# Kernel tuning notes

Measured on AMD Instinct MI355X. Metric: run time of the kernel, lower is better.

Reference implementation:

```python
import jax, jax.numpy as jnp
import numpy as np

HID = 256
IN_DIM = 256
OUT_DIM = 10
L_CYCLES = 6
H_CYCLES = 3
BATCH = 131072
LN_EPS = 1e-5


def _layernorm(v, w, b):
    mu = jnp.mean(v, axis=-1, keepdims=True)
    var = jnp.mean(jnp.square(v - mu), axis=-1, keepdims=True)
    return (v - mu) * jax.lax.rsqrt(var + LN_EPS) * w + b


def setup_inputs() -> dict:
    key = jax.random.key(0)
    ks = jax.random.split(key, 12)
    s = lambda fan_in: 1.0 / np.sqrt(fan_in)
    inp = {
        "x": jax.random.normal(ks[0], (BATCH, IN_DIM), dtype=jnp.float32),
        "W_in": jax.random.uniform(ks[1], (IN_DIM, HID), jnp.float32, -s(IN_DIM), s(IN_DIM)),
        "b_in": jnp.zeros((HID,), jnp.float32),
        "y_init": jax.random.normal(ks[2], (1, HID), dtype=jnp.float32) * 0.02,
        "W_up": jax.random.uniform(ks[3], (HID, 4 * HID), jnp.float32, -s(HID), s(HID)),
        "b_up": jnp.zeros((4 * HID,), jnp.float32),
        "W_down": jax.random.uniform(ks[4], (4 * HID, HID), jnp.float32, -s(4 * HID), s(4 * HID)),
        "b_down": jnp.zeros((HID,), jnp.float32),
        "ln_w": jnp.ones((HID,), jnp.float32),
        "ln_b": jnp.zeros((HID,), jnp.float32),
        "W_comb": jax.random.uniform(ks[5], (2 * HID, HID), jnp.float32, -s(2 * HID), s(2 * HID)),
        "b_comb": jnp.zeros((HID,), jnp.float32),
        "W_yt": jax.random.uniform(ks[6], (HID, HID), jnp.float32, -s(HID), s(HID)),
        "b_yt": jnp.zeros((HID,), jnp.float32),
        "W_head": jax.random.uniform(ks[7], (HID, OUT_DIM), jnp.float32, -s(HID), s(HID)),
        "b_head": jnp.zeros((OUT_DIM,), jnp.float32),
    }
    return inp


def reference(x, W_in, b_in, y_init, W_up, b_up, W_down, b_down, ln_w, ln_b,
              W_comb, b_comb, W_yt, b_yt, W_head, b_head):
    z = x @ W_in + b_in                      # [B, H]
    y = jnp.broadcast_to(y_init, (x.shape[0], HID))
    for _ in range(H_CYCLES):
        for _ in range(L_CYCLES):
            h = jax.nn.gelu(z @ W_up + b_up, approximate=False)
            h = h @ W_down + b_down
            z = _layernorm(z + h, ln_w, ln_b)
        combined = jnp.concatenate([z, y], axis=-1)   # [B, 2H]
        h = jax.nn.gelu(combined @ W_comb + b_comb, approximate=False)
        y = y + h @ W_yt + b_yt
    return y @ W_head + b_head
```

## Files before the change

### kernel.cpp

```cpp
#include <hip/hip_runtime.h>

typedef _Float16 h16;
typedef h16 h16x8 __attribute__((ext_vector_type(8)));
typedef float f32x4 __attribute__((ext_vector_type(4)));

#define MFMA16(a, b, c) __builtin_amdgcn_mfma_f32_16x16x32_f16(a, b, c, 0, 0, 0)

typedef __attribute__((address_space(1))) const char gconst_char;
typedef __attribute__((address_space(3))) char lds_char;
#define GL_LDS16(g, l) __builtin_amdgcn_global_load_lds((gconst_char*)(g), (lds_char*)(l), 16, 0, 0)

#define WIN_OFF   0
#define WIN_CSH   17408
#define WUP_OFF   (WIN_OFF + 8 * WIN_CSH)
#define WUP_CSH   17408
#define WDN_OFF   (WUP_OFF + 32 * WUP_CSH)
#define WDN_CSH   20480
#define WCOMB_OFF (WDN_OFF + 32 * WDN_CSH)
#define WCOMB_CSH 33792
#define WYT_OFF   (WCOMB_OFF + 8 * WCOMB_CSH)
#define WYT_CSH   20480
#define WHEAD_OFF (WYT_OFF + 8 * WYT_CSH)
#define WHEAD_SZ  9216
#define ZY_OFF    (WHEAD_OFF + WHEAD_SZ)
#define ZY_BYTES  (131072UL * 512UL * 2UL)

#define L_WUP0 0
#define L_WUP1 17408
#define L_WDN0 34816
#define L_WDN1 55296
#define L_HS   75776
#define L_BUP  96256
#define L_BDN  100352
#define L_LNW  101376
#define L_LNB  102400
#define SMEM_MEGA 103424

#define C_WC0 0
#define C_WC1 33792
#define C_WY0 67584
#define C_WY1 88064
#define C_GS  108544
#define C_BC  129024
#define C_BY  130048
#define SMEM_COMB 131072

#define SMEM_HEAD 9216

__device__ __forceinline__ void stage_calls(const char* src, char* dst, int calls, int wave,
                                            int nw, int lane) {
  for (int i = wave; i < calls; i += nw)
    GL_LDS16(src + i * 1024 + lane * 16, dst + i * 1024);
}

__device__ __forceinline__ float gelu_f(float x) {
  float t = x * (1.5957691216f + 0.0713548354f * x * x);
  float e = __expf(-t);
  return x * __builtin_amdgcn_rcpf(1.0f + e);
}

__global__ void prepA_kernel(const float* __restrict__ src, h16* __restrict__ dst,
                             int K, int KPp, int CHN, int Nsrc, int CSHh, int tot) {
  for (int d = blockIdx.x * 256 + threadIdx.x; d < tot; d += gridDim.x * 256) {
    int chunk = d / CSHh, r = d % CSHh;
    float v = 0.0f;
    if (r < CHN * KPp) {
      int nl = r / KPp, k = r % KPp;
      int n = chunk * CHN + nl;
      if (k < K && n < Nsrc) v = src[(long)k * Nsrc + n];
    }
    dst[d] = (h16)v;
  }
}
__global__ void prepB_kernel(const float* __restrict__ src, h16* __restrict__ dst,
                             int Kc, int KP2p, int N, int CSHh, int tot) {
  for (int d = blockIdx.x * 256 + threadIdx.x; d < tot; d += gridDim.x * 256) {
    int chunk = d / CSHh, r = d % CSHh;
    float v = 0.0f;
    if (r < N * KP2p) {
      int n = r / KP2p, kp = r % KP2p;
      if (kp < Kc) v = src[(long)(chunk * Kc + kp) * N + n];
    }
    dst[d] = (h16)v;
  }
}

__global__ __launch_bounds__(512) void mega_kernel(
    const float* x, h16* zy,
    const char* __restrict__ winP, const char* __restrict__ wupP, const char* __restrict__ wdnP,
    const float* __restrict__ b_in, const float* __restrict__ b_up,
    const float* __restrict__ b_down, const float* __restrict__ ln_w,
    const float* __restrict__ ln_b, int first) {
  extern __shared__ char smem[];
  const int tid = threadIdx.x, wave = tid >> 6, lane = tid & 63;
  const int q = lane >> 4, c = lane & 15;
  const long m0 = (long)blockIdx.x * 256 + wave * 32;

  float* bupL = (float*)(smem + L_BUP);
  float* bdnL = (float*)(smem + L_BDN);
  float* lnwL = (float*)(smem + L_LNW);
  float* lnbL = (float*)(smem + L_LNB);
  for (int i = tid; i < 1024; i += 512) bupL[i] = b_up[i];
  if (tid < 256) { bdnL[tid] = b_down[tid]; lnwL[tid] = ln_w[tid]; lnbL[tid] = ln_b[tid]; }

  f32x4 acc2[2][16];
  h16x8 az[2][8];
  h16* hsH = (h16*)(smem + L_HS + wave * 2560);
  const f32x4 vzero = {0.0f, 0.0f, 0.0f, 0.0f};

  if (first) {
#pragma unroll
    for (int rt = 0; rt < 2; ++rt)
#pragma unroll
      for (int kk = 0; kk < 8; ++kk) {
        const float* p = x + (m0 + rt * 16 + c) * 256 + kk * 32 + q * 8;
        f32x4 u0 = *(const f32x4*)p;
        f32x4 u1 = *(const f32x4*)(p + 4);
        h16x8 a;
        a[0] = (h16)u0[0]; a[1] = (h16)u0[1]; a[2] = (h16)u0[2]; a[3] = (h16)u0[3];
        a[4] = (h16)u1[0]; a[5] = (h16)u1[1]; a[6] = (h16)u1[2]; a[7] = (h16)u1[3];
        az[rt][kk] = a;
      }
#pragma unroll
    for (int rt = 0; rt < 2; ++rt)
#pragma unroll
      for (int nt = 0; nt < 16; ++nt) acc2[rt][nt] = vzero;

    stage_calls(winP, smem + L_WUP0, 17, wave, 8, lane);
    __syncthreads();
#pragma unroll
    for (int ncI = 0; ncI < 8; ++ncI) {
      if (ncI < 7)
        stage_calls(winP + (ncI + 1) * WIN_CSH, smem + (((ncI + 1) & 1) ? L_WUP1 : L_WUP0),
                    17, wave, 8, lane);
      const char* wb = smem + ((ncI & 1) ? L_WUP1 : L_WUP0);
#pragma unroll
      for (int kk = 0; kk < 8; ++kk)
#pragma unroll
        for (int nt = 0; nt < 2; ++nt) {
          h16x8 b = *(const h16x8*)(wb + ((nt * 16 + c) * 264 + kk * 32 + q * 8) * 2);
#pragma unroll
          for (int rt = 0; rt < 2; ++rt)
            acc2[rt][ncI * 2 + nt] = MFMA16(az[rt][kk], b, acc2[rt][ncI * 2 + nt]);
        }
      __syncthreads();
    }
#pragma unroll
    for (int nt = 0; nt < 16; ++nt) {
      float bi = b_in[nt * 16 + c];
#pragma unroll
      for (int rt = 0; rt < 2; ++rt)
#pragma unroll
        for (int r = 0; r < 4; ++r) acc2[rt][nt][r] += bi;
    }
  } else {
#pragma unroll
    for (int rt = 0; rt < 2; ++rt)
#pragma unroll
      for (int kk = 0; kk < 8; ++kk)
        az[rt][kk] = *(const h16x8*)(zy + (m0 + rt * 16 + c) * 512 + kk * 32 + q * 8);
#pragma unroll
    for (int rt = 0; rt < 2; ++rt)
#pragma unroll
      for (int nt = 0; nt < 16; ++nt)
#pragma unroll
        for (int r = 0; r < 4; ++r)
          acc2[rt][nt][r] = (float)zy[(m0 + rt * 16 + q * 4 + r) * 512 + nt * 16 + c];
  }

  for (int it = 0; it < 6; ++it) {
    if (it > 0 || first) {
      h16* zth = (h16*)(smem + wave * 8448);
#pragma unroll
      for (int rt = 0; rt < 2; ++rt) {
#pragma unroll
        for (int nt = 0; nt < 16; ++nt)
#pragma unroll
          for (int r = 0; r < 4; ++r)
            zth[(q * 4 + r) * 264 + nt * 16 + c] = (h16)acc2[rt][nt][r];
#pragma unroll
        for (int kk = 0; kk < 8; ++kk)
          az[rt][kk] = *(const h16x8*)(zth + c * 264 + kk * 32 + q * 8);
      }
    }
    __syncthreads();
    stage_calls(wupP, smem + L_WUP0, 17, wave, 8, lane);
    stage_calls(wdnP, smem + L_WDN0, 20, wave, 8, lane);
    __syncthreads();

    for (int nc = 0; nc < 32; ++nc) {
      if (nc < 31) {
        int nb = (nc + 1) & 1;
        stage_calls(wupP + (nc + 1) * WUP_CSH, smem + (nb ? L_WUP1 : L_WUP0), 17, wave, 8, lane);
        stage_calls(wdnP + (nc + 1) * WDN_CSH, smem + (nb ? L_WDN1 : L_WDN0), 20, wave, 8, lane);
      }
      const char* wub = smem + ((nc & 1) ? L_WUP1 : L_WUP0);
      const char* wdb = smem + ((nc & 1) ? L_WDN1 : L_WDN0);

      f32x4 acc1[2][2];
      acc1[0][0] = vzero; acc1[0][1] = vzero; acc1[1][0] = vzero; acc1[1][1] = vzero;
#pragma unroll
      for (int kk = 0; kk < 8; ++kk)
#pragma unroll
        for (int nt = 0; nt < 2; ++nt) {
          h16x8 b = *(const h16x8*)(wub + ((nt * 16 + c) * 264 + kk * 32 + q * 8) * 2);
#pragma unroll
          for (int rt = 0; rt < 2; ++rt) acc1[rt][nt] = MFMA16(az[rt][kk], b, acc1[rt][nt]);
        }
#pragma unroll
      for (int rt = 0; rt < 2; ++rt)
#pragma unroll
        for (int nt = 0; nt < 2; ++nt) {
          float bu = bupL[nc * 32 + nt * 16 + c];
#pragma unroll
          for (int r = 0; r < 4; ++r) {
            float g = gelu_f(acc1[rt][nt][r] + bu);
            hsH[(rt * 16 + q * 4 + r) * 40 + nt * 16 + c] = (h16)g;
          }
        }
      h16x8 ah[2];
#pragma unroll
      for (int rt = 0; rt < 2; ++rt)
        ah[rt] = *(const h16x8*)(hsH + (rt * 16 + c) * 40 + q * 8);
#pragma unroll
      for (int nt = 0; nt < 16; ++nt) {
        h16x8 b = *(const h16x8*)(wdb + ((nt * 16 + c) * 40 + q * 8) * 2);
#pragma unroll
        for (int rt = 0; rt < 2; ++rt) acc2[rt][nt] = MFMA16(ah[rt], b, acc2[rt][nt]);
      }
      __syncthreads();
    }

#pragma unroll
    for (int rt = 0; rt < 2; ++rt) {
      float sum[4] = {0, 0, 0, 0}, sq[4] = {0, 0, 0, 0};
#pragma unroll
      for (int nt = 0; nt < 16; ++nt) {
        float bd = bdnL[nt * 16 + c];
#pragma unroll
        for (int r = 0; r < 4; ++r) {
          float v = acc2[rt][nt][r] + bd;
          acc2[rt][nt][r] = v;
          sum[r] += v;
          sq[r] += v * v;
        }
      }
#pragma unroll
      for (int r = 0; r < 4; ++r)
#pragma unroll
        for (int m = 1; m < 16; m <<= 1) {
          sum[r] += __shfl_xor(sum[r], m, 16);
          sq[r] += __shfl_xor(sq[r], m, 16);
        }
      float mu[4], rs[4];
#pragma unroll
      for (int r = 0; r < 4; ++r) {
        mu[r] = sum[r] * (1.0f / 256.0f);
        float var = sq[r] * (1.0f / 256.0f) - mu[r] * mu[r];
        rs[r] = __builtin_amdgcn_rsqf(var + 1e-5f);
      }
#pragma unroll
      for (int nt = 0; nt < 16; ++nt) {
        float w = lnwL[nt * 16 + c], bb = lnbL[nt * 16 + c];
#pragma unroll
        for (int r = 0; r < 4; ++r)
          acc2[rt][nt][r] = (acc2[rt][nt][r] - mu[r]) * rs[r] * w + bb;
      }
    }
  }

#pragma unroll
  for (int rt = 0; rt < 2; ++rt)
#pragma unroll
    for (int nt = 0; nt < 16; ++nt)
#pragma unroll
      for (int r = 0; r < 4; ++r)
        zy[(m0 + rt * 16 + q * 4 + r) * 512 + nt * 16 + c] = (h16)acc2[rt][nt][r];
}

__global__ __launch_bounds__(512) void comb_kernel(
    h16* zy, const char* __restrict__ wcP, const char* __restrict__ wytP,
    const float* __restrict__ b_comb, const float* __restrict__ b_yt,
    const float* __restrict__ y_init, int first) {
  extern __shared__ char smem[];
  const int tid = threadIdx.x, wave = tid >> 6, lane = tid & 63;
  const int q = lane >> 4, c = lane & 15;
  const long m0 = (long)blockIdx.x * 256 + wave * 32;

  float* bcL = (float*)(smem + C_BC);
  float* byL = (float*)(smem + C_BY);
  if (tid < 256) { bcL[tid] = b_comb[tid]; byL[tid] = b_yt[tid]; }

  f32x4 acc2[2][16];
  if (first) {
#pragma unroll
    for (int nt = 0; nt < 16; ++nt) {
      float yv = y_init[nt * 16 + c];
#pragma unroll
      for (int rt = 0; rt < 2; ++rt)
#pragma unroll
        for (int r = 0; r < 4; ++r) acc2[rt][nt][r] = yv;
    }
  } else {
#pragma unroll
    for (int rt = 0; rt < 2; ++rt)
#pragma unroll
      for (int nt = 0; nt < 16; ++nt)
#pragma unroll
        for (int r = 0; r < 4; ++r)
          acc2[rt][nt][r] = (float)zy[(m0 + rt * 16 + q * 4 + r) * 512 + 256 + nt * 16 + c];
  }
  h16* gsH = (h16*)(smem + C_GS + wave * 2560);
  const f32x4 vzero = {0.0f, 0.0f, 0.0f, 0.0f};

  stage_calls(wcP, smem + C_WC0, 33, wave, 8, lane);
  stage_calls(wytP, smem + C_WY0, 20, wave, 8, lane);
  __syncthreads();

  for (int nc = 0; nc < 8; ++nc) {
    if (nc < 7) {
      int nb = (nc + 1) & 1;
      stage_calls(wcP + (nc + 1) * WCOMB_CSH, smem + (nb ? C_WC1 : C_WC0), 33, wave, 8, lane);
      stage_calls(wytP + (nc + 1) * WYT_CSH, smem + (nb ? C_WY1 : C_WY0), 20, wave, 8, lane);
    }
    const char* wcb = smem + ((nc & 1) ? C_WC1 : C_WC0);
    const char* wyb = smem + ((nc & 1) ? C_WY1 : C_WY0);

    f32x4 acc1[2][2];
    acc1[0][0] = vzero; acc1[0][1] = vzero; acc1[1][0] = vzero; acc1[1][1] = vzero;
#pragma unroll
    for (int kk = 0; kk < 16; ++kk) {
      h16x8 a[2];
#pragma unroll
      for (int rt = 0; rt < 2; ++rt)
        a[rt] = *(const h16x8*)(zy + (m0 + rt * 16 + c) * 512 + kk * 32 + q * 8);
#pragma unroll
      for (int nt = 0; nt < 2; ++nt) {
        h16x8 b = *(const h16x8*)(wcb + ((nt * 16 + c) * 520 + kk * 32 + q * 8) * 2);
#pragma unroll
        for (int rt = 0; rt < 2; ++rt) acc1[rt][nt] = MFMA16(a[rt], b, acc1[rt][nt]);
      }
    }
#pragma unroll
    for (int rt = 0; rt < 2; ++rt)
#pragma unroll
      for (int nt = 0; nt < 2; ++nt) {
        float bc = bcL[nc * 32 + nt * 16 + c];
#pragma unroll
        for (int r = 0; r < 4; ++r) {
          float g = gelu_f(acc1[rt][nt][r] + bc);
          gsH[(rt * 16 + q * 4 + r) * 40 + nt * 16 + c] = (h16)g;
        }
      }
    h16x8 ah[2];
#pragma unroll
    for (int rt = 0; rt < 2; ++rt)
      ah[rt] = *(const h16x8*)(gsH + (rt * 16 + c) * 40 + q * 8);
#pragma unroll
    for (int nt = 0; nt < 16; ++nt) {
      h16x8 b = *(const h16x8*)(wyb + ((nt * 16 + c) * 40 + q * 8) * 2);
#pragma unroll
      for (int rt = 0; rt < 2; ++rt) acc2[rt][nt] = MFMA16(ah[rt], b, acc2[rt][nt]);
    }
    __syncthreads();
  }

#pragma unroll
  for (int nt = 0; nt < 16; ++nt) {
    float by = byL[nt * 16 + c];
#pragma unroll
    for (int rt = 0; rt < 2; ++rt)
#pragma unroll
      for (int r = 0; r < 4; ++r)
        zy[(m0 + rt * 16 + q * 4 + r) * 512 + 256 + nt * 16 + c] = (h16)(acc2[rt][nt][r] + by);
  }
}

__global__ __launch_bounds__(256) void head_kernel(const h16* zy, const char* __restrict__ whP,
                                                   const float* __restrict__ b_head,
                                                   float* __restrict__ out) {
  extern __shared__ char smem[];
  const int tid = threadIdx.x, wave = tid >> 6, lane = tid & 63;
  const int q = lane >> 4, c = lane & 15;
  const long m0 = (long)blockIdx.x * 128 + wave * 32;

  stage_calls(whP, smem, 9, wave, 4, lane);
  __syncthreads();

  f32x4 acc[2];
  const f32x4 vzero = {0.0f, 0.0f, 0.0f, 0.0f};
  acc[0] = vzero; acc[1] = vzero;
#pragma unroll
  for (int kk = 0; kk < 8; ++kk) {
    h16x8 b = *(const h16x8*)(smem + (c * 264 + kk * 32 + q * 8) * 2);
#pragma unroll
    for (int rt = 0; rt < 2; ++rt) {
      h16x8 a = *(const h16x8*)(zy + (m0 + rt * 16 + c) * 512 + 256 + kk * 32 + q * 8);
      acc[rt] = MFMA16(a, b, acc[rt]);
    }
  }
  if (c < 10) {
    float bh = b_head[c];
#pragma unroll
    for (int rt = 0; rt < 2; ++rt)
#pragma unroll
      for (int r = 0; r < 4; ++r)
        out[(m0 + rt * 16 + q * 4 + r) * 10 + c] = acc[rt][r] + bh;
  }
}

extern "C" void kernel_launch(void* const* d_in, const int* in_sizes, int n_in, void* d_out,
                              int out_size, void* d_ws, size_t ws_size, hipStream_t stream) {
  (void)in_sizes; (void)n_in; (void)out_size;
  const float* x      = (const float*)d_in[0];
  const float* W_in   = (const float*)d_in[1];
  const float* b_in   = (const float*)d_in[2];
  const float* y_init = (const float*)d_in[3];
  const float* W_up   = (const float*)d_in[4];
  const float* b_up   = (const float*)d_in[5];
  const float* W_down = (const float*)d_in[6];
  const float* b_down = (const float*)d_in[7];
  const float* ln_w   = (const float*)d_in[8];
  const float* ln_b   = (const float*)d_in[9];
  const float* W_comb = (const float*)d_in[10];
  const float* b_comb = (const float*)d_in[11];
  const float* W_yt   = (const float*)d_in[12];
  const float* b_yt   = (const float*)d_in[13];
  const float* W_head = (const float*)d_in[14];
  const float* b_head = (const float*)d_in[15];

  char* ws = (char*)d_ws;
  h16* winP   = (h16*)(ws + WIN_OFF);
  h16* wupP   = (h16*)(ws + WUP_OFF);
  h16* wdnP   = (h16*)(ws + WDN_OFF);
  h16* wcombP = (h16*)(ws + WCOMB_OFF);
  h16* wytP   = (h16*)(ws + WYT_OFF);
  h16* wheadP = (h16*)(ws + WHEAD_OFF);
  h16* zy = (ws_size >= (size_t)ZY_OFF + ZY_BYTES) ? (h16*)(ws + ZY_OFF) : (h16*)d_in[0];

  hipFuncSetAttribute((const void*)mega_kernel, hipFuncAttributeMaxDynamicSharedMemorySize,
                      SMEM_MEGA);
  hipFuncSetAttribute((const void*)comb_kernel, hipFuncAttributeMaxDynamicSharedMemorySize,
                      SMEM_COMB);

  {
    int tot;
    tot = 8 * (WIN_CSH / 2);
    prepA_kernel<<<dim3((tot + 255) / 256), dim3(256), 0, stream>>>(W_in, winP, 256, 264, 32, 256, WIN_CSH / 2, tot);
    tot = 32 * (WUP_CSH / 2);
    prepA_kernel<<<dim3((tot + 255) / 256), dim3(256), 0, stream>>>(W_up, wupP, 256, 264, 32, 1024, WUP_CSH / 2, tot);
    tot = 8 * (WCOMB_CSH / 2);
    prepA_kernel<<<dim3((tot + 255) / 256), dim3(256), 0, stream>>>(W_comb, wcombP, 512, 520, 32, 256, WCOMB_CSH / 2, tot);
    tot = WHEAD_SZ / 2;
    prepA_kernel<<<dim3((tot + 255) / 256), dim3(256), 0, stream>>>(W_head, wheadP, 256, 264, 16, 10, WHEAD_SZ / 2, tot);
    tot = 32 * (WDN_CSH / 2);
    prepB_kernel<<<dim3((tot + 255) / 256), dim3(256), 0, stream>>>(W_down, wdnP, 32, 40, 256, WDN_CSH / 2, tot);
    tot = 8 * (WYT_CSH / 2);
    prepB_kernel<<<dim3((tot + 255) / 256), dim3(256), 0, stream>>>(W_yt, wytP, 32, 40, 256, WYT_CSH / 2, tot);
  }

  for (int h = 0; h < 3; ++h) {
    mega_kernel<<<dim3(512), dim3(512), SMEM_MEGA, stream>>>(
        x, zy, (const char*)winP, (const char*)wupP, (const char*)wdnP, b_in, b_up, b_down,
        ln_w, ln_b, (h == 0) ? 1 : 0);
    comb_kernel<<<dim3(512), dim3(512), SMEM_COMB, stream>>>(
        zy, (const char*)wcombP, (const char*)wytP, b_comb, b_yt, y_init, (h == 0) ? 1 : 0);
  }
  head_kernel<<<dim3(1024), dim3(256), SMEM_HEAD, stream>>>(zy, (const char*)wheadP, b_head,
                                                            (float*)d_out);
}
```

Before: 4.068 ms.

## Pre-swizzle weights into MFMA fragment order and pipeline staging across iterations

```diff
diff --git a/kernel.cpp b/kernel.cpp
--- a/kernel.cpp
+++ b/kernel.cpp
@@ -10,42 +10,43 @@
 typedef __attribute__((address_space(3))) char lds_char;
 #define GL_LDS16(g, l) __builtin_amdgcn_global_load_lds((gconst_char*)(g), (lds_char*)(l), 16, 0, 0)
 
+#define WIN_CSH   16384
 #define WIN_OFF   0
-#define WIN_CSH   17408
-#define WUP_OFF   (WIN_OFF + 8 * WIN_CSH)
-#define WUP_CSH   17408
-#define WDN_OFF   (WUP_OFF + 32 * WUP_CSH)
-#define WDN_CSH   20480
-#define WCOMB_OFF (WDN_OFF + 32 * WDN_CSH)
-#define WCOMB_CSH 33792
-#define WYT_OFF   (WCOMB_OFF + 8 * WCOMB_CSH)
-#define WYT_CSH   20480
-#define WHEAD_OFF (WYT_OFF + 8 * WYT_CSH)
-#define WHEAD_SZ  9216
-#define ZY_OFF    (WHEAD_OFF + WHEAD_SZ)
+#define WUP_CSH   16384
+#define WUP_OFF   131072
+#define WDN_CSH   16384
+#define WDN_OFF   655360
+#define WCOMB_CSH 32768
+#define WCOMB_OFF 1179648
+#define WYT_CSH   16384
+#define WYT_OFF   1441792
+#define WHEAD_SZ  8192
+#define WHEAD_OFF 1572864
+#define ZY_OFF    1581056
 #define ZY_BYTES  (131072UL * 512UL * 2UL)
 
 #define L_WUP0 0
-#define L_WUP1 17408
-#define L_WDN0 34816
-#define L_WDN1 55296
-#define L_HS   75776
-#define L_BUP  96256
-#define L_BDN  100352
-#define L_LNW  101376
-#define L_LNB  102400
-#define SMEM_MEGA 103424
+#define L_WUP1 16384
+#define L_WDN0 32768
+#define L_WDN1 49152
+#define L_HS   65536
+#define L_ZT   86016
+#define L_BUP  153600
+#define L_BDN  157696
+#define L_LNW  158720
+#define L_LNB  159744
+#define SMEM_MEGA 160768
 
 #define C_WC0 0
-#define C_WC1 33792
-#define C_WY0 67584
-#define C_WY1 88064
-#define C_GS  108544
-#define C_BC  129024
-#define C_BY  130048
-#define SMEM_COMB 131072
-
-#define SMEM_HEAD 9216
+#define C_WC1 32768
+#define C_WY0 65536
+#define C_WY1 81920
+#define C_GS  98304
+#define C_BC  118784
+#define C_BY  119808
+#define SMEM_COMB 120832
+
+#define SMEM_HEAD 8192
 
 __device__ __forceinline__ void stage_calls(const char* src, char* dst, int calls, int wave,
                                             int nw, int lane) {
@@ -59,29 +60,32 @@
   return x * __builtin_amdgcn_rcpf(1.0f + e);
 }
 
-__global__ void prepA_kernel(const float* __restrict__ src, h16* __restrict__ dst,
-                             int K, int KPp, int CHN, int Nsrc, int CSHh, int tot) {
+__global__ void prepC_kernel(const float* __restrict__ src, h16* __restrict__ dst,
+                             int Nsrc, int CSHh, int tot) {
   for (int d = blockIdx.x * 256 + threadIdx.x; d < tot; d += gridDim.x * 256) {
     int chunk = d / CSHh, r = d % CSHh;
-    float v = 0.0f;
-    if (r < CHN * KPp) {
-      int nl = r / KPp, k = r % KPp;
-      int n = chunk * CHN + nl;
-      if (k < K && n < Nsrc) v = src[(long)k * Nsrc + n];
-    }
-    dst[d] = (h16)v;
-  }
-}
-__global__ void prepB_kernel(const float* __restrict__ src, h16* __restrict__ dst,
-                             int Kc, int KP2p, int N, int CSHh, int tot) {
+    int frag = r >> 9, lane = (r >> 3) & 63, j = r & 7;
+    int kk = frag >> 1, nt = frag & 1, q = lane >> 4, c = lane & 15;
+    int k = kk * 32 + q * 8 + j;
+    int n = chunk * 32 + nt * 16 + c;
+    dst[d] = (h16)src[(long)k * Nsrc + n];
+  }
+}
+__global__ void prepD_kernel(const float* __restrict__ src, h16* __restrict__ dst, int tot) {
   for (int d = blockIdx.x * 256 + threadIdx.x; d < tot; d += gridDim.x * 256) {
-    int chunk = d / CSHh, r = d % CSHh;
-    float v = 0.0f;
-    if (r < N * KP2p) {
-      int n = r / KP2p, kp = r % KP2p;
-      if (kp < Kc) v = src[(long)(chunk * Kc + kp) * N + n];
-    }
-    dst[d] = (h16)v;
+    int chunk = d >> 13, r = d & 8191;
+    int nt = r >> 9, lane = (r >> 3) & 63, j = r & 7;
+    int q = lane >> 4, c = lane & 15;
+    int k = chunk * 32 + q * 8 + j;
+    dst[d] = (h16)src[(long)k * 256 + nt * 16 + c];
+  }
+}
+__global__ void prepH_kernel(const float* __restrict__ src, h16* __restrict__ dst) {
+  for (int d = blockIdx.x * 256 + threadIdx.x; d < 4096; d += gridDim.x * 256) {
+    int kk = d >> 9, lane = (d >> 3) & 63, j = d & 7;
+    int q = lane >> 4, c = lane & 15;
+    int k = kk * 32 + q * 8 + j;
+    dst[d] = (h16)((c < 10) ? src[k * 10 + c] : 0.0f);
   }
 }
 
@@ -90,10 +94,11 @@
     const char* __restrict__ winP, const char* __restrict__ wupP, const char* __restrict__ wdnP,
     const float* __restrict__ b_in, const float* __restrict__ b_up,
     const float* __restrict__ b_down, const float* __restrict__ ln_w,
-    const float* __restrict__ ln_b, int first) {
+    const float* __restrict__ ln_b, const float* __restrict__ y_init, int first) {
   extern __shared__ char smem[];
   const int tid = threadIdx.x, wave = tid >> 6, lane = tid & 63;
   const int q = lane >> 4, c = lane & 15;
+  const int lane16 = lane << 4;
   const long m0 = (long)blockIdx.x * 256 + wave * 32;
 
   float* bupL = (float*)(smem + L_BUP);
@@ -106,6 +111,7 @@
   f32x4 acc2[2][16];
   h16x8 az[2][8];
   h16* hsH = (h16*)(smem + L_HS + wave * 2560);
+  h16* zth = (h16*)(smem + L_ZT + wave * 8448);
   const f32x4 vzero = {0.0f, 0.0f, 0.0f, 0.0f};
 
   if (first) {
@@ -126,22 +132,21 @@
 #pragma unroll
       for (int nt = 0; nt < 16; ++nt) acc2[rt][nt] = vzero;
 
-    stage_calls(winP, smem + L_WUP0, 17, wave, 8, lane);
+    stage_calls(winP, smem + L_WUP0, 16, wave, 8, lane);
     __syncthreads();
 #pragma unroll
     for (int ncI = 0; ncI < 8; ++ncI) {
       if (ncI < 7)
         stage_calls(winP + (ncI + 1) * WIN_CSH, smem + (((ncI + 1) & 1) ? L_WUP1 : L_WUP0),
-                    17, wave, 8, lane);
+                    16, wave, 8, lane);
       const char* wb = smem + ((ncI & 1) ? L_WUP1 : L_WUP0);
 #pragma unroll
       for (int kk = 0; kk < 8; ++kk)
 #pragma unroll
         for (int nt = 0; nt < 2; ++nt) {
-          h16x8 b = *(const h16x8*)(wb + ((nt * 16 + c) * 264 + kk * 32 + q * 8) * 2);
-#pragma unroll
-          for (int rt = 0; rt < 2; ++rt)
-            acc2[rt][ncI * 2 + nt] = MFMA16(az[rt][kk], b, acc2[rt][ncI * 2 + nt]);
+          h16x8 b = *(const h16x8*)(wb + ((kk * 2 + nt) << 10) + lane16);
+          acc2[0][ncI * 2 + nt] = MFMA16(az[0][kk], b, acc2[0][ncI * 2 + nt]);
+          acc2[1][ncI * 2 + nt] = MFMA16(az[1][kk], b, acc2[1][ncI * 2 + nt]);
         }
       __syncthreads();
     }
@@ -153,24 +158,43 @@
 #pragma unroll
         for (int r = 0; r < 4; ++r) acc2[rt][nt][r] += bi;
     }
+#pragma unroll
+    for (int kk = 0; kk < 8; ++kk) {
+      const float* p = y_init + kk * 32 + q * 8;
+      f32x4 u0 = *(const f32x4*)p;
+      f32x4 u1 = *(const f32x4*)(p + 4);
+      h16x8 a;
+      a[0] = (h16)u0[0]; a[1] = (h16)u0[1]; a[2] = (h16)u0[2]; a[3] = (h16)u0[3];
+      a[4] = (h16)u1[0]; a[5] = (h16)u1[1]; a[6] = (h16)u1[2]; a[7] = (h16)u1[3];
+#pragma unroll
+      for (int rt = 0; rt < 2; ++rt)
+        *(h16x8*)(zy + (m0 + rt * 16 + c) * 512 + 256 + kk * 32 + q * 8) = a;
+    }
+    stage_calls(wupP, smem + L_WUP0, 16, wave, 8, lane);
+    stage_calls(wdnP, smem + L_WDN0, 16, wave, 8, lane);
   } else {
+    stage_calls(wupP, smem + L_WUP0, 16, wave, 8, lane);
+    stage_calls(wdnP, smem + L_WDN0, 16, wave, 8, lane);
 #pragma unroll
     for (int rt = 0; rt < 2; ++rt)
 #pragma unroll
       for (int kk = 0; kk < 8; ++kk)
         az[rt][kk] = *(const h16x8*)(zy + (m0 + rt * 16 + c) * 512 + kk * 32 + q * 8);
 #pragma unroll
-    for (int rt = 0; rt < 2; ++rt)
+    for (int rt = 0; rt < 2; ++rt) {
+#pragma unroll
+      for (int kk = 0; kk < 8; ++kk)
+        *(h16x8*)(zth + c * 264 + kk * 32 + q * 8) = az[rt][kk];
 #pragma unroll
       for (int nt = 0; nt < 16; ++nt)
 #pragma unroll
         for (int r = 0; r < 4; ++r)
-          acc2[rt][nt][r] = (float)zy[(m0 + rt * 16 + q * 4 + r) * 512 + nt * 16 + c];
+          acc2[rt][nt][r] = (float)zth[(q * 4 + r) * 264 + nt * 16 + c];
+    }
   }
 
   for (int it = 0; it < 6; ++it) {
     if (it > 0 || first) {
-      h16* zth = (h16*)(smem + wave * 8448);
 #pragma unroll
       for (int rt = 0; rt < 2; ++rt) {
 #pragma unroll
@@ -183,19 +207,19 @@
           az[rt][kk] = *(const h16x8*)(zth + c * 264 + kk * 32 + q * 8);
       }
     }
-    __syncthreads();
-    stage_calls(wupP, smem + L_WUP0, 17, wave, 8, lane);
-    stage_calls(wdnP, smem + L_WDN0, 20, wave, 8, lane);
-    __syncthreads();
 
     for (int nc = 0; nc < 32; ++nc) {
-      if (nc < 31) {
-        int nb = (nc + 1) & 1;
-        stage_calls(wupP + (nc + 1) * WUP_CSH, smem + (nb ? L_WUP1 : L_WUP0), 17, wave, 8, lane);
-        stage_calls(wdnP + (nc + 1) * WDN_CSH, smem + (nb ? L_WDN1 : L_WDN0), 20, wave, 8, lane);
-      }
-      const char* wub = smem + ((nc & 1) ? L_WUP1 : L_WUP0);
-      const char* wdb = smem + ((nc & 1) ? L_WDN1 : L_WDN0);
+      const int tc = it * 32 + nc;
+      __syncthreads();
+      if (tc < 191) {
+        const int nxt = (nc + 1) & 31;
+        char* wu = smem + (((tc + 1) & 1) ? L_WUP1 : L_WUP0);
+        char* wd = smem + (((tc + 1) & 1) ? L_WDN1 : L_WDN0);
+        stage_calls(wupP + nxt * WUP_CSH, wu, 16, wave, 8, lane);
+        stage_calls(wdnP + nxt * WDN_CSH, wd, 16, wave, 8, lane);
+      }
+      const char* wub = smem + ((tc & 1) ? L_WUP1 : L_WUP0);
+      const char* wdb = smem + ((tc & 1) ? L_WDN1 : L_WDN0);
 
       f32x4 acc1[2][2];
       acc1[0][0] = vzero; acc1[0][1] = vzero; acc1[1][0] = vzero; acc1[1][1] = vzero;
@@ -203,9 +227,9 @@
       for (int kk = 0; kk < 8; ++kk)
 #pragma unroll
         for (int nt = 0; nt < 2; ++nt) {
-          h16x8 b = *(const h16x8*)(wub + ((nt * 16 + c) * 264 + kk * 32 + q * 8) * 2);
-#pragma unroll
-          for (int rt = 0; rt < 2; ++rt) acc1[rt][nt] = MFMA16(az[rt][kk], b, acc1[rt][nt]);
+          h16x8 b = *(const h16x8*)(wub + ((kk * 2 + nt) << 10) + lane16);
+          acc1[0][nt] = MFMA16(az[0][kk], b, acc1[0][nt]);
+          acc1[1][nt] = MFMA16(az[1][kk], b, acc1[1][nt]);
         }
 #pragma unroll
       for (int rt = 0; rt < 2; ++rt)
@@ -218,17 +242,14 @@
             hsH[(rt * 16 + q * 4 + r) * 40 + nt * 16 + c] = (h16)g;
           }
         }
-      h16x8 ah[2];
-#pragma unroll
-      for (int rt = 0; rt < 2; ++rt)
-        ah[rt] = *(const h16x8*)(hsH + (rt * 16 + c) * 40 + q * 8);
+      h16x8 ah0 = *(const h16x8*)(hsH + c * 40 + q * 8);
+      h16x8 ah1 = *(const h16x8*)(hsH + (16 + c) * 40 + q * 8);
 #pragma unroll
       for (int nt = 0; nt < 16; ++nt) {
-        h16x8 b = *(const h16x8*)(wdb + ((nt * 16 + c) * 40 + q * 8) * 2);
-#pragma unroll
-        for (int rt = 0; rt < 2; ++rt) acc2[rt][nt] = MFMA16(ah[rt], b, acc2[rt][nt]);
-      }
-      __syncthreads();
+        h16x8 b = *(const h16x8*)(wdb + (nt << 10) + lane16);
+        acc2[0][nt] = MFMA16(ah0, b, acc2[0][nt]);
+        acc2[1][nt] = MFMA16(ah1, b, acc2[1][nt]);
+      }
     }
 
 #pragma unroll
@@ -270,12 +291,17 @@
   }
 
 #pragma unroll
-  for (int rt = 0; rt < 2; ++rt)
+  for (int rt = 0; rt < 2; ++rt) {
 #pragma unroll
     for (int nt = 0; nt < 16; ++nt)
 #pragma unroll
       for (int r = 0; r < 4; ++r)
-        zy[(m0 + rt * 16 + q * 4 + r) * 512 + nt * 16 + c] = (h16)acc2[rt][nt][r];
+        zth[(q * 4 + r) * 264 + nt * 16 + c] = (h16)acc2[rt][nt][r];
+#pragma unroll
+    for (int kk = 0; kk < 8; ++kk)
+      *(h16x8*)(zy + (m0 + rt * 16 + c) * 512 + kk * 32 + q * 8) =
+          *(const h16x8*)(zth + c * 264 + kk * 32 + q * 8);
+  }
 }
 
 __global__ __launch_bounds__(512) void comb_kernel(
@@ -285,6 +311,7 @@
   extern __shared__ char smem[];
   const int tid = threadIdx.x, wave = tid >> 6, lane = tid & 63;
   const int q = lane >> 4, c = lane & 15;
+  const int lane16 = lane << 4;
   const long m0 = (long)blockIdx.x * 256 + wave * 32;
 
   float* bcL = (float*)(smem + C_BC);
@@ -302,26 +329,34 @@
         for (int r = 0; r < 4; ++r) acc2[rt][nt][r] = yv;
     }
   } else {
-#pragma unroll
-    for (int rt = 0; rt < 2; ++rt)
+    h16* zth = (h16*)(smem + wave * 8448);
+#pragma unroll
+    for (int rt = 0; rt < 2; ++rt) {
+#pragma unroll
+      for (int kk = 0; kk < 8; ++kk)
+        *(h16x8*)(zth + c * 264 + kk * 32 + q * 8) =
+            *(const h16x8*)(zy + (m0 + rt * 16 + c) * 512 + 256 + kk * 32 + q * 8);
 #pragma unroll
       for (int nt = 0; nt < 16; ++nt)
 #pragma unroll
         for (int r = 0; r < 4; ++r)
-          acc2[rt][nt][r] = (float)zy[(m0 + rt * 16 + q * 4 + r) * 512 + 256 + nt * 16 + c];
-  }
+          acc2[rt][nt][r] = (float)zth[(q * 4 + r) * 264 + nt * 16 + c];
+    }
+  }
+  __syncthreads();
+
   h16* gsH = (h16*)(smem + C_GS + wave * 2560);
   const f32x4 vzero = {0.0f, 0.0f, 0.0f, 0.0f};
 
-  stage_calls(wcP, smem + C_WC0, 33, wave, 8, lane);
-  stage_calls(wytP, smem + C_WY0, 20, wave, 8, lane);
-  __syncthreads();
+  stage_calls(wcP, smem + C_WC0, 32, wave, 8, lane);
+  stage_calls(wytP, smem + C_WY0, 16, wave, 8, lane);
 
   for (int nc = 0; nc < 8; ++nc) {
+    __syncthreads();
     if (nc < 7) {
       int nb = (nc + 1) & 1;
-      stage_calls(wcP + (nc + 1) * WCOMB_CSH, smem + (nb ? C_WC1 : C_WC0), 33, wave, 8, lane);
-      stage_calls(wytP + (nc + 1) * WYT_CSH, smem + (nb ? C_WY1 : C_WY0), 20, wave, 8, lane);
+      stage_calls(wcP + (nc + 1) * WCOMB_CSH, smem + (nb ? C_WC1 : C_WC0), 32, wave, 8, lane);
+      stage_calls(wytP + (nc + 1) * WYT_CSH, smem + (nb ? C_WY1 : C_WY0), 16, wave, 8, lane);
     }
     const char* wcb = smem + ((nc & 1) ? C_WC1 : C_WC0);
     const char* wyb = smem + ((nc & 1) ? C_WY1 : C_WY0);
@@ -330,15 +365,13 @@
     acc1[0][0] = vzero; acc1[0][1] = vzero; acc1[1][0] = vzero; acc1[1][1] = vzero;
 #pragma unroll
     for (int kk = 0; kk < 16; ++kk) {
-      h16x8 a[2];
-#pragma unroll
-      for (int rt = 0; rt < 2; ++rt)
-        a[rt] = *(const h16x8*)(zy + (m0 + rt * 16 + c) * 512 + kk * 32 + q * 8);
+      h16x8 a0 = *(const h16x8*)(zy + (m0 + c) * 512 + kk * 32 + q * 8);
+      h16x8 a1 = *(const h16x8*)(zy + (m0 + 16 + c) * 512 + kk * 32 + q * 8);
 #pragma unroll
       for (int nt = 0; nt < 2; ++nt) {
-        h16x8 b = *(const h16x8*)(wcb + ((nt * 16 + c) * 520 + kk * 32 + q * 8) * 2);
-#pragma unroll
-        for (int rt = 0; rt < 2; ++rt) acc1[rt][nt] = MFMA16(a[rt], b, acc1[rt][nt]);
+        h16x8 b = *(const h16x8*)(wcb + ((kk * 2 + nt) << 10) + lane16);
+        acc1[0][nt] = MFMA16(a0, b, acc1[0][nt]);
+        acc1[1][nt] = MFMA16(a1, b, acc1[1][nt]);
       }
     }
 #pragma unroll
@@ -352,27 +385,31 @@
           gsH[(rt * 16 + q * 4 + r) * 40 + nt * 16 + c] = (h16)g;
         }
       }
-    h16x8 ah[2];
-#pragma unroll
-    for (int rt = 0; rt < 2; ++rt)
-      ah[rt] = *(const h16x8*)(gsH + (rt * 16 + c) * 40 + q * 8);
+    h16x8 ah0 = *(const h16x8*)(gsH + c * 40 + q * 8);
+    h16x8 ah1 = *(const h16x8*)(gsH + (16 + c) * 40 + q * 8);
 #pragma unroll
     for (int nt = 0; nt < 16; ++nt) {
-      h16x8 b = *(const h16x8*)(wyb + ((nt * 16 + c) * 40 + q * 8) * 2);
-#pragma unroll
-      for (int rt = 0; rt < 2; ++rt) acc2[rt][nt] = MFMA16(ah[rt], b, acc2[rt][nt]);
-    }
-    __syncthreads();
-  }
-
-#pragma unroll
-  for (int nt = 0; nt < 16; ++nt) {
-    float by = byL[nt * 16 + c];
-#pragma unroll
-    for (int rt = 0; rt < 2; ++rt)
+      h16x8 b = *(const h16x8*)(wyb + (nt << 10) + lane16);
+      acc2[0][nt] = MFMA16(ah0, b, acc2[0][nt]);
+      acc2[1][nt] = MFMA16(ah1, b, acc2[1][nt]);
+    }
+  }
+
+  __syncthreads();
+  h16* zth = (h16*)(smem + wave * 8448);
+#pragma unroll
+  for (int rt = 0; rt < 2; ++rt) {
+#pragma unroll
+    for (int nt = 0; nt < 16; ++nt) {
+      float by = byL[nt * 16 + c];
 #pragma unroll
       for (int r = 0; r < 4; ++r)
-        zy[(m0 + rt * 16 + q * 4 + r) * 512 + 256 + nt * 16 + c] = (h16)(acc2[rt][nt][r] + by);
+        zth[(q * 4 + r) * 264 + nt * 16 + c] = (h16)(acc2[rt][nt][r] + by);
+    }
+#pragma unroll
+    for (int kk = 0; kk < 8; ++kk)
+      *(h16x8*)(zy + (m0 + rt * 16 + c) * 512 + 256 + kk * 32 + q * 8) =
+          *(const h16x8*)(zth + c * 264 + kk * 32 + q * 8);
   }
 }
 
@@ -382,9 +419,10 @@
   extern __shared__ char smem[];
   const int tid = threadIdx.x, wave = tid >> 6, lane = tid & 63;
   const int q = lane >> 4, c = lane & 15;
+  const int lane16 = lane << 4;
   const long m0 = (long)blockIdx.x * 128 + wave * 32;
 
-  stage_calls(whP, smem, 9, wave, 4, lane);
+  stage_calls(whP, smem, 8, wave, 4, lane);
   __syncthreads();
 
   f32x4 acc[2];
@@ -392,7 +430,7 @@
   acc[0] = vzero; acc[1] = vzero;
 #pragma unroll
   for (int kk = 0; kk < 8; ++kk) {
-    h16x8 b = *(const h16x8*)(smem + (c * 264 + kk * 32 + q * 8) * 2);
+    h16x8 b = *(const h16x8*)(smem + (kk << 10) + lane16);
 #pragma unroll
     for (int rt = 0; rt < 2; ++rt) {
       h16x8 a = *(const h16x8*)(zy + (m0 + rt * 16 + c) * 512 + 256 + kk * 32 + q * 8);
@@ -446,23 +484,22 @@
   {
     int tot;
     tot = 8 * (WIN_CSH / 2);
-    prepA_kernel<<<dim3((tot + 255) / 256), dim3(256), 0, stream>>>(W_in, winP, 256, 264, 32, 256, WIN_CSH / 2, tot);
+    prepC_kernel<<<dim3((tot + 255) / 256), dim3(256), 0, stream>>>(W_in, winP, 256, WIN_CSH / 2, tot);
     tot = 32 * (WUP_CSH / 2);
-    prepA_kernel<<<dim3((tot + 255) / 256), dim3(256), 0, stream>>>(W_up, wupP, 256, 264, 32, 1024, WUP_CSH / 2, tot);
+    prepC_kernel<<<dim3((tot + 255) / 256), dim3(256), 0, stream>>>(W_up, wupP, 1024, WUP_CSH / 2, tot);
     tot = 8 * (WCOMB_CSH / 2);
-    prepA_kernel<<<dim3((tot + 255) / 256), dim3(256), 0, stream>>>(W_comb, wcombP, 512, 520, 32, 256, WCOMB_CSH / 2, tot);
-    tot = WHEAD_SZ / 2;
-    prepA_kernel<<<dim3((tot + 255) / 256), dim3(256), 0, stream>>>(W_head, wheadP, 256, 264, 16, 10, WHEAD_SZ / 2, tot);
+    prepC_kernel<<<dim3((tot + 255) / 256), dim3(256), 0, stream>>>(W_comb, wcombP, 256, WCOMB_CSH / 2, tot);
     tot = 32 * (WDN_CSH / 2);
-    prepB_kernel<<<dim3((tot + 255) / 256), dim3(256), 0, stream>>>(W_down, wdnP, 32, 40, 256, WDN_CSH / 2, tot);
+    prepD_kernel<<<dim3((tot + 255) / 256), dim3(256), 0, stream>>>(W_down, wdnP, tot);
     tot = 8 * (WYT_CSH / 2);
-    prepB_kernel<<<dim3((tot + 255) / 256), dim3(256), 0, stream>>>(W_yt, wytP, 32, 40, 256, WYT_CSH / 2, tot);
+    prepD_kernel<<<dim3((tot + 255) / 256), dim3(256), 0, stream>>>(W_yt, wytP, tot);
+    prepH_kernel<<<dim3(16), dim3(256), 0, stream>>>(W_head, wheadP);
   }
 
   for (int h = 0; h < 3; ++h) {
     mega_kernel<<<dim3(512), dim3(512), SMEM_MEGA, stream>>>(
         x, zy, (const char*)winP, (const char*)wupP, (const char*)wdnP, b_in, b_up, b_down,
-        ln_w, ln_b, (h == 0) ? 1 : 0);
+        ln_w, ln_b, y_init, (h == 0) ? 1 : 0);
     comb_kernel<<<dim3(512), dim3(512), SMEM_COMB, stream>>>(
         zy, (const char*)wcombP, (const char*)wytP, b_comb, b_yt, y_init, (h == 0) ? 1 : 0);
   }
```

After: 4.658 ms. 1.15x slower.
